# Kernel tuning notes

Hardware: AMD Instinct MI355X
Metric: run time of the kernel (lower is better)

The kernel has to match this reference:

```python
import jax, jax.numpy as jnp
import numpy as np

ALPHA = 2.0    # ATan surrogate sharpness
V_TH = 1.0     # LIF firing threshold
TAU = 2.0      # LIF membrane time constant
BN_EPS = 1e-5
NUM_HEADS = 8

@jax.custom_vjp
def spike(u):
    return (u >= 0.0).astype(u.dtype)

def _spike_fwd(u):
    return spike(u), u

def _spike_bwd(u, g):
    s = (jnp.pi / 2.0) * ALPHA * u
    return (g * (ALPHA / 2.0) / (1.0 + s * s),)

spike.defvjp(_spike_fwd, _spike_bwd)

def lif(x):
    # x: (T, ...) -> binary spikes, multi-step LIF with hard reset
    def step(mem, xt):
        mem = mem + (xt - mem) / TAU
        s = spike(mem - V_TH)
        return mem * (1.0 - s), s
    _, out = jax.lax.scan(step, jnp.zeros_like(x[0]), x)
    return out

def bn_eval(y, bn):
    g, be, m, v = bn[0], bn[1], bn[2], bn[3]  # each (C,)
    return (y - m) * jax.lax.rsqrt(v + BN_EPS) * g + be

def linear_bn_lif(x, W, b, bn):
    # x: (T,B,N,C); W: (C_out, C_in) torch convention
    y = jnp.einsum('tbnc,dc->tbnd', x, W) + b
    return lif(bn_eval(y, bn))

def setup_inputs() -> dict:
    key = jax.random.key(0)
    ks = jax.random.split(key, 6)
    T, B, N, C = 4, 8, 1024, 512
    scale = 1.0 / np.sqrt(C)
    x = jax.random.normal(ks[0], (T, B, N, C), dtype=jnp.float32)
    Wq = jax.random.normal(ks[1], (C, C), dtype=jnp.float32) * scale
    Wk = jax.random.normal(ks[2], (C, C), dtype=jnp.float32) * scale
    Wv = jax.random.normal(ks[3], (C, C), dtype=jnp.float32) * scale
    Wp = jax.random.normal(ks[4], (C, C), dtype=jnp.float32) * scale
    zeros = jnp.zeros((C,), dtype=jnp.float32)
    ones = jnp.ones((C,), dtype=jnp.float32)
    # bn_params[l] = (gamma, beta, running_mean, running_var) for q_bn,k_bn,v_bn,proj_bn
    bn_one = jnp.stack([ones, zeros, zeros, ones])  # (4, C)
    bn_params = jnp.tile(bn_one[None], (4, 1, 1))   # (4, 4, C)
    return {"x": x, "Wq": Wq, "bq": zeros, "Wk": Wk, "bk": zeros,
            "Wv": Wv, "bv": zeros, "Wp": Wp, "bp": zeros, "bn_params": bn_params}

def reference(x, Wq, bq, Wk, bk, Wv, bv, Wp, bp, bn_params):
    T, B, N, C = x.shape
    H = NUM_HEADS
    D = C // H
    q = linear_bn_lif(x, Wq, bq, bn_params[0])
    k = linear_bn_lif(x, Wk, bk, bn_params[1])
    v = linear_bn_lif(x, Wv, bv, bn_params[2])
    # (T,B,N,C) -> (T,B,H,N,D)
    q = q.reshape(T, B, N, H, D).transpose(0, 1, 3, 2, 4)
    k = k.reshape(T, B, N, H, D).transpose(0, 1, 3, 2, 4)
    v = v.reshape(T, B, N, H, D).transpose(0, 1, 3, 2, 4)
    # attention_linear variant: kv = (k^T @ v) / n; y = q @ kv
    # SparseMatmul's tile-sparsity fallback computes the same dense matmul math.
    kv = jnp.einsum('tbhnd,tbhne->tbhde', k, v) / float(N)
    y = jnp.einsum('tbhnd,tbhde->tbhne', q, kv)
    y = y.transpose(0, 1, 3, 2, 4).reshape(T, B, N, C)
    y = lif(y)  # attn_lif
    # final projection: proj -> proj_bn -> proj_lif
    y = jnp.einsum('tbnc,dc->tbnd', y, Wp) + bp
    y = bn_eval(y, bn_params[3])
    y = lif(y)  # proj_lif
    return y
```

## Files before the change

### kernel.cpp

```cpp
#include <hip/hip_runtime.h>
#include <hip/hip_bf16.h>

constexpr int T_ = 4, B_ = 8, N_ = 1024, C_ = 512, H_ = 8, D_ = 64;
constexpr int M_ = 8192;
constexpr int MT_ = 32768;
constexpr int K_ = 512;

#define TAU_INV 0.5f
#define V_TH    1.0f
#define BN_EPS  1e-5f

__device__ __forceinline__ void ld4(const float* p, float* d) {
  const float4 v = *(const float4*)p;
  d[0] = v.x; d[1] = v.y; d[2] = v.z; d[3] = v.w;
}
__device__ __forceinline__ void ld4(const __hip_bfloat16* p, float* d) {
  const ushort4 u = *(const ushort4*)p;
  d[0] = __bfloat162float(*(const __hip_bfloat16*)&u.x);
  d[1] = __bfloat162float(*(const __hip_bfloat16*)&u.y);
  d[2] = __bfloat162float(*(const __hip_bfloat16*)&u.z);
  d[3] = __bfloat162float(*(const __hip_bfloat16*)&u.w);
}
__device__ __forceinline__ void st4(__hip_bfloat16* p, const float* s) {
  ushort4 u;
  *(__hip_bfloat16*)&u.x = __float2bfloat16(s[0]);
  *(__hip_bfloat16*)&u.y = __float2bfloat16(s[1]);
  *(__hip_bfloat16*)&u.z = __float2bfloat16(s[2]);
  *(__hip_bfloat16*)&u.w = __float2bfloat16(s[3]);
  *(ushort4*)p = u;
}
__device__ __forceinline__ void st4(float* p, const float* s) {
  *(float4*)p = make_float4(s[0], s[1], s[2], s[3]);
}

__device__ __forceinline__ void dma16(const void* g, void* l) {
  __builtin_amdgcn_global_load_lds(
      (const __attribute__((address_space(1))) unsigned int*)g,
      (__attribute__((address_space(3))) unsigned int*)l, 16, 0, 0);
}

struct WPtrs { const float* W[4]; };

__global__ __launch_bounds__(256) void transpose_w(WPtrs wp, float* __restrict__ Wt)
{
  __shared__ float tile[32][33];
  const int w = blockIdx.z;
  const float* __restrict__ W = wp.W[w];
  float* __restrict__ dst = Wt + (size_t)w * K_ * C_;
  const int k0 = blockIdx.x * 32, d0 = blockIdx.y * 32;
  const int tx = threadIdx.x, ty = threadIdx.y;
#pragma unroll
  for (int i = 0; i < 32; i += 8)
    tile[ty + i][tx] = W[(size_t)(d0 + ty + i) * K_ + k0 + tx];
  __syncthreads();
#pragma unroll
  for (int i = 0; i < 32; i += 8)
    dst[(size_t)(k0 + ty + i) * C_ + d0 + tx] = tile[tx][ty + i];
}

__global__ __launch_bounds__(256) void transpose_x(
    const float* __restrict__ x, float* __restrict__ XT)
{
  __shared__ float tile[32][132];
  const int bk = blockIdx.x * 32, bm = blockIdx.y * 32;
  const int tx = threadIdx.x & 31, ty = threadIdx.x >> 5;
#pragma unroll
  for (int t = 0; t < T_; ++t)
#pragma unroll
    for (int i = 0; i < 4; ++i) {
      const int m = ty + 8 * i;
      tile[tx][m * 4 + t] = x[((size_t)t * M_ + bm + m) * K_ + bk + tx];
    }
  __syncthreads();
  const int k = threadIdx.x >> 3, q = threadIdx.x & 7;
#pragma unroll
  for (int u = 0; u < 4; ++u)
    st4(&XT[(size_t)(bk + k) * MT_ + bm * 4 + q * 16 + u * 4],
        &tile[k][q * 16 + u * 4]);
}

template <typename TIn, typename TOut>
struct GArgs {
  const TIn* AT;
  const float* Wt[3];
  const float* bias[3];
  const float* bn[3];
  TOut* S[3];
};

template <typename TIn, typename TOut>
__global__ __launch_bounds__(256, 2) void gemm_lif(GArgs<TIn, TOut> args)
{
  constexpr int BK = 32;
  constexpr bool BF = (sizeof(TIn) == 2);
  __shared__ __align__(16) TIn  As[BK * 128];
  __shared__ __align__(16) float Bs[BK * 256];

  const int z = blockIdx.z;
  const TIn*   __restrict__ AT   = args.AT;
  const float* __restrict__ Wt   = args.Wt[z];
  const float* __restrict__ bias = args.bias[z];
  const float* __restrict__ bnp  = args.bn[z];
  TOut*        __restrict__ S    = args.S[z];

  const int tid  = threadIdx.x;
  const int lane = tid & 63;
  const int wave = __builtin_amdgcn_readfirstlane(tid >> 6);
  const int tx = tid & 15, ty = tid >> 4;
  const int bm_m = blockIdx.y * 32;
  const int bm4  = bm_m * 4;
  const int bn0  = blockIdx.x * 256;

  float acc[2][4][4][4];
#pragma unroll
  for (int g = 0; g < 2; ++g)
#pragma unroll
    for (int h = 0; h < 4; ++h)
#pragma unroll
      for (int i = 0; i < 4; ++i)
#pragma unroll
        for (int j = 0; j < 4; ++j) acc[g][h][i][j] = 0.0f;

  for (int k0 = 0; k0 < K_; k0 += BK) {
    if constexpr (!BF) {
#pragma unroll
      for (int c = 0; c < 4; ++c) {
        const int ins = wave * 4 + c;
        const int kk = ins * 2 + (lane >> 5);
        dma16(AT + (size_t)(k0 + kk) * MT_ + bm4 + (lane & 31) * 4,
              (void*)((float*)As + ins * 256));
      }
    } else {
#pragma unroll
      for (int c = 0; c < 2; ++c) {
        const int ins = wave * 2 + c;
        const int kk = ins * 4 + (lane >> 4);
        dma16(AT + (size_t)(k0 + kk) * MT_ + bm4 + (lane & 15) * 8,
              (void*)((TIn*)As + ins * 512));
      }
    }
#pragma unroll
    for (int c = 0; c < 8; ++c) {
      const int ins = wave * 8 + c;
      dma16(Wt + (size_t)(k0 + ins) * C_ + bn0 + lane * 4,
            (void*)(Bs + ins * 256));
    }
    __syncthreads();

#pragma unroll
    for (int kk = 0; kk < BK; ++kk) {
      float a[2][4], b[4][4];
#pragma unroll
      for (int g = 0; g < 2; ++g)
        ld4((const TIn*)As + kk * 128 + ty * 4 + 64 * g, a[g]);
#pragma unroll
      for (int h = 0; h < 4; ++h)
        ld4(Bs + kk * 256 + tx * 4 + 64 * h, b[h]);
#pragma unroll
      for (int g = 0; g < 2; ++g)
#pragma unroll
        for (int h = 0; h < 4; ++h)
#pragma unroll
          for (int i = 0; i < 4; ++i)
#pragma unroll
            for (int j = 0; j < 4; ++j)
              acc[g][h][i][j] += a[g][i] * b[h][j];
    }
    __syncthreads();
  }

#pragma unroll
  for (int h = 0; h < 4; ++h) {
    const int d = bn0 + tx * 4 + 64 * h;
    float bi[4], gg[4], be[4], mu[4], vv[4];
    ld4(&bias[d], bi);
    ld4(&bnp[d], gg);
    ld4(&bnp[C_ + d], be);
    ld4(&bnp[2 * C_ + d], mu);
    ld4(&bnp[3 * C_ + d], vv);
    float inv[4];
#pragma unroll
    for (int j = 0; j < 4; ++j) inv[j] = 1.0f / sqrtf(vv[j] + BN_EPS);
#pragma unroll
    for (int g = 0; g < 2; ++g) {
      const int m = bm_m + ty + 16 * g;
      float sv[4][4];
#pragma unroll
      for (int j = 0; j < 4; ++j) {
        float mm = 0.0f;
#pragma unroll
        for (int t = 0; t < 4; ++t) {
          float y = acc[g][h][t][j] + bi[j];
          y = (y - mu[j]) * inv[j] * gg[j] + be[j];
          float m2 = mm + (y - mm) * TAU_INV;
          float s = (m2 - V_TH >= 0.0f) ? 1.0f : 0.0f;
          sv[t][j] = s;
          mm = (s != 0.0f) ? 0.0f : m2;
        }
      }
#pragma unroll
      for (int t = 0; t < 4; ++t)
        st4(&S[((size_t)t * M_ + m) * C_ + d], sv[t]);
    }
  }
}

__global__ __launch_bounds__(256) void lif_T(
    const float* __restrict__ Y, __hip_bfloat16* __restrict__ AT)
{
  __shared__ __hip_bfloat16 lds[64][72];
  const int bm = blockIdx.x * 16, bc = blockIdx.y * 64;
  const int tid = threadIdx.x;
  const int mm = tid >> 4, c4 = (tid & 15) * 4;
  float mem[4] = {0.0f, 0.0f, 0.0f, 0.0f};
#pragma unroll
  for (int t = 0; t < T_; ++t) {
    float y[4];
    ld4(&Y[((size_t)t * M_ + bm + mm) * C_ + bc + c4], y);
#pragma unroll
    for (int j = 0; j < 4; ++j) {
      float m2 = mem[j] + (y[j] - mem[j]) * TAU_INV;
      float s = (m2 - V_TH >= 0.0f) ? 1.0f : 0.0f;
      lds[c4 + j][mm * 4 + t] = __float2bfloat16(s);
      mem[j] = (s != 0.0f) ? 0.0f : m2;
    }
  }
  __syncthreads();
  const int c = tid >> 2, q = tid & 3;
  *(uint4*)(AT + (size_t)(bc + c) * MT_ + bm * 4 + q * 16) =
      *(const uint4*)&lds[c][q * 16];
}

__global__ __launch_bounds__(256) void attn_kernel(
    const __hip_bfloat16* __restrict__ Q,
    const __hip_bfloat16* __restrict__ Kk,
    const __hip_bfloat16* __restrict__ V,
    float* __restrict__ Y)
{
  __shared__ float s1[64][65];
  __shared__ float s2[64][65];
  __shared__ float kv[64][65];
  const int tid = threadIdx.x;
  const int h = blockIdx.x, b = blockIdx.y, t = blockIdx.z;
  const size_t base = ((size_t)t * B_ + b) * (size_t)N_ * C_ + (size_t)h * D_;
  const int d0 = (tid >> 4) * 4;
  const int e0 = (tid & 15) * 4;

  float acc[4][4];
#pragma unroll
  for (int i = 0; i < 4; ++i)
#pragma unroll
    for (int j = 0; j < 4; ++j) acc[i][j] = 0.0f;

  for (int nc = 0; nc < N_; nc += 64) {
#pragma unroll
    for (int i = 0; i < 16; ++i) {
      int idx = tid + i * 256;
      int r = idx >> 6, c = idx & 63;
      s1[r][c] = __bfloat162float(Kk[base + (size_t)(nc + r) * C_ + c]);
      s2[r][c] = __bfloat162float(V[base + (size_t)(nc + r) * C_ + c]);
    }
    __syncthreads();
#pragma unroll
    for (int nn = 0; nn < 64; ++nn) {
      float a[4], bb[4];
#pragma unroll
      for (int i = 0; i < 4; ++i) a[i] = s1[nn][d0 + i];
#pragma unroll
      for (int j = 0; j < 4; ++j) bb[j] = s2[nn][e0 + j];
#pragma unroll
      for (int i = 0; i < 4; ++i)
#pragma unroll
        for (int j = 0; j < 4; ++j) acc[i][j] += a[i] * bb[j];
    }
    __syncthreads();
  }
#pragma unroll
  for (int i = 0; i < 4; ++i)
#pragma unroll
    for (int j = 0; j < 4; ++j)
      kv[d0 + i][e0 + j] = acc[i][j] * (1.0f / (float)N_);
  __syncthreads();

  for (int rc = 0; rc < N_; rc += 64) {
#pragma unroll
    for (int i = 0; i < 16; ++i) {
      int idx = tid + i * 256;
      int r = idx >> 6, c = idx & 63;
      s1[r][c] = __bfloat162float(Q[base + (size_t)(rc + r) * C_ + c]);
    }
    __syncthreads();
    float o[4][4];
#pragma unroll
    for (int i = 0; i < 4; ++i)
#pragma unroll
      for (int j = 0; j < 4; ++j) o[i][j] = 0.0f;
#pragma unroll
    for (int d = 0; d < 64; ++d) {
      float a[4], bb[4];
#pragma unroll
      for (int i = 0; i < 4; ++i) a[i] = s1[d0 + i][d];
#pragma unroll
      for (int j = 0; j < 4; ++j) bb[j] = kv[d][e0 + j];
#pragma unroll
      for (int i = 0; i < 4; ++i)
#pragma unroll
        for (int j = 0; j < 4; ++j) o[i][j] += a[i] * bb[j];
    }
#pragma unroll
    for (int i = 0; i < 4; ++i)
#pragma unroll
      for (int j = 0; j < 4; ++j)
        Y[base + (size_t)(rc + d0 + i) * C_ + e0 + j] = o[i][j];
    __syncthreads();
  }
}

extern "C" void kernel_launch(void* const* d_in, const int* in_sizes, int n_in,
                              void* d_out, int out_size, void* d_ws, size_t ws_size,
                              hipStream_t stream)
{
  const float* x   = (const float*)d_in[0];
  const float* Wq  = (const float*)d_in[1];
  const float* bq  = (const float*)d_in[2];
  const float* Wk  = (const float*)d_in[3];
  const float* bk  = (const float*)d_in[4];
  const float* Wv  = (const float*)d_in[5];
  const float* bv  = (const float*)d_in[6];
  const float* Wp  = (const float*)d_in[7];
  const float* bp  = (const float*)d_in[8];
  const float* bnp = (const float*)d_in[9];
  float* out = (float*)d_out;

  char* ws = (char*)d_ws;
  float* XT = (float*)ws;  ws += (size_t)K_ * MT_ * sizeof(float);
  float* Wt = (float*)ws;  ws += (size_t)4 * K_ * C_ * sizeof(float);
  __hip_bfloat16* q_s = (__hip_bfloat16*)ws; ws += (size_t)MT_ * C_ * 2;
  __hip_bfloat16* k_s = (__hip_bfloat16*)ws; ws += (size_t)MT_ * C_ * 2;
  __hip_bfloat16* v_s = (__hip_bfloat16*)ws; ws += (size_t)MT_ * C_ * 2;
  float* Y = XT;
  __hip_bfloat16* aT = q_s;

  WPtrs wp; wp.W[0] = Wq; wp.W[1] = Wk; wp.W[2] = Wv; wp.W[3] = Wp;
  transpose_w<<<dim3(K_ / 32, C_ / 32, 4), dim3(32, 8), 0, stream>>>(wp, Wt);
  transpose_x<<<dim3(K_ / 32, M_ / 32), 256, 0, stream>>>(x, XT);

  GArgs<float, __hip_bfloat16> qa;
  qa.AT = XT;
  qa.Wt[0] = Wt; qa.Wt[1] = Wt + (size_t)K_ * C_; qa.Wt[2] = Wt + (size_t)2 * K_ * C_;
  qa.bias[0] = bq; qa.bias[1] = bk; qa.bias[2] = bv;
  qa.bn[0] = bnp + 0 * 4 * C_;
  qa.bn[1] = bnp + 1 * 4 * C_;
  qa.bn[2] = bnp + 2 * 4 * C_;
  qa.S[0] = q_s; qa.S[1] = k_s; qa.S[2] = v_s;
  gemm_lif<float, __hip_bfloat16>
      <<<dim3(C_ / 256, M_ / 32, 3), 256, 0, stream>>>(qa);

  attn_kernel<<<dim3(H_, B_, T_), 256, 0, stream>>>(q_s, k_s, v_s, Y);
  lif_T<<<dim3(M_ / 16, C_ / 64), 256, 0, stream>>>(Y, aT);

  GArgs<__hip_bfloat16, float> pa;
  pa.AT = aT;
  pa.Wt[0] = Wt + (size_t)3 * K_ * C_;
  pa.bias[0] = bp;
  pa.bn[0] = bnp + 3 * 4 * C_;
  pa.S[0] = out;
  gemm_lif<__hip_bfloat16, float>
      <<<dim3(C_ / 256, M_ / 32, 1), 256, 0, stream>>>(pa);
}
```

Before: 984.4 us.

## Double-buffer GEMM shared tiles and vectorize attention bf16 loads

```diff
diff --git a/kernel.cpp b/kernel.cpp
--- a/kernel.cpp
+++ b/kernel.cpp
@@ -91,10 +91,11 @@
 template <typename TIn, typename TOut>
 __global__ __launch_bounds__(256, 2) void gemm_lif(GArgs<TIn, TOut> args)
 {
-  constexpr int BK = 32;
+  constexpr int BK = 16;
+  constexpr int NIT = K_ / BK;
   constexpr bool BF = (sizeof(TIn) == 2);
-  __shared__ __align__(16) TIn  As[BK * 128];
-  __shared__ __align__(16) float Bs[BK * 256];
+  __shared__ __align__(16) TIn  As[2][BK * 128];
+  __shared__ __align__(16) float Bs[2][BK * 256];
 
   const int z = blockIdx.z;
   const TIn*   __restrict__ AT   = args.AT;
@@ -121,41 +122,51 @@
 #pragma unroll
         for (int j = 0; j < 4; ++j) acc[g][h][i][j] = 0.0f;
 
-  for (int k0 = 0; k0 < K_; k0 += BK) {
+  auto stageA = [&](int it) {
+    const int k0 = it * BK;
+    TIn* dst = As[it & 1];
     if constexpr (!BF) {
 #pragma unroll
-      for (int c = 0; c < 4; ++c) {
-        const int ins = wave * 4 + c;
+      for (int c = 0; c < 2; ++c) {
+        const int ins = wave * 2 + c;
         const int kk = ins * 2 + (lane >> 5);
         dma16(AT + (size_t)(k0 + kk) * MT_ + bm4 + (lane & 31) * 4,
-              (void*)((float*)As + ins * 256));
+              (void*)((float*)dst + ins * 256));
       }
     } else {
-#pragma unroll
-      for (int c = 0; c < 2; ++c) {
-        const int ins = wave * 2 + c;
-        const int kk = ins * 4 + (lane >> 4);
-        dma16(AT + (size_t)(k0 + kk) * MT_ + bm4 + (lane & 15) * 8,
-              (void*)((TIn*)As + ins * 512));
-      }
-    }
-#pragma unroll
-    for (int c = 0; c < 8; ++c) {
-      const int ins = wave * 8 + c;
+      const int kk = wave * 4 + (lane >> 4);
+      dma16(AT + (size_t)(k0 + kk) * MT_ + bm4 + (lane & 15) * 8,
+            (void*)((TIn*)dst + wave * 512));
+    }
+  };
+  auto stageB = [&](int it) {
+    const int k0 = it * BK;
+    float* dst = Bs[it & 1];
+#pragma unroll
+    for (int c = 0; c < 4; ++c) {
+      const int ins = wave * 4 + c;
       dma16(Wt + (size_t)(k0 + ins) * C_ + bn0 + lane * 4,
-            (void*)(Bs + ins * 256));
-    }
-    __syncthreads();
+            (void*)(dst + ins * 256));
+    }
+  };
+
+  stageA(0); stageB(0);
+  __syncthreads();
+
+  for (int it = 0; it < NIT; ++it) {
+    if (it + 1 < NIT) { stageA(it + 1); stageB(it + 1); }
+    const TIn*   Ac = As[it & 1];
+    const float* Bc = Bs[it & 1];
 
 #pragma unroll
     for (int kk = 0; kk < BK; ++kk) {
       float a[2][4], b[4][4];
 #pragma unroll
       for (int g = 0; g < 2; ++g)
-        ld4((const TIn*)As + kk * 128 + ty * 4 + 64 * g, a[g]);
+        ld4(Ac + kk * 128 + ty * 4 + 64 * g, a[g]);
 #pragma unroll
       for (int h = 0; h < 4; ++h)
-        ld4(Bs + kk * 256 + tx * 4 + 64 * h, b[h]);
+        ld4(Bc + kk * 256 + tx * 4 + 64 * h, b[h]);
 #pragma unroll
       for (int g = 0; g < 2; ++g)
 #pragma unroll
@@ -254,11 +265,14 @@
 
   for (int nc = 0; nc < N_; nc += 64) {
 #pragma unroll
-    for (int i = 0; i < 16; ++i) {
-      int idx = tid + i * 256;
-      int r = idx >> 6, c = idx & 63;
-      s1[r][c] = __bfloat162float(Kk[base + (size_t)(nc + r) * C_ + c]);
-      s2[r][c] = __bfloat162float(V[base + (size_t)(nc + r) * C_ + c]);
+    for (int i = 0; i < 4; ++i) {
+      const int idx = tid + i * 256;
+      const int r = idx >> 4, c4 = (idx & 15) * 4;
+      float fk[4], fv[4];
+      ld4(&Kk[base + (size_t)(nc + r) * C_ + c4], fk);
+      ld4(&V [base + (size_t)(nc + r) * C_ + c4], fv);
+#pragma unroll
+      for (int j = 0; j < 4; ++j) { s1[r][c4 + j] = fk[j]; s2[r][c4 + j] = fv[j]; }
     }
     __syncthreads();
 #pragma unroll
@@ -284,10 +298,13 @@
 
   for (int rc = 0; rc < N_; rc += 64) {
 #pragma unroll
-    for (int i = 0; i < 16; ++i) {
-      int idx = tid + i * 256;
-      int r = idx >> 6, c = idx & 63;
-      s1[r][c] = __bfloat162float(Q[base + (size_t)(rc + r) * C_ + c]);
+    for (int i = 0; i < 4; ++i) {
+      const int idx = tid + i * 256;
+      const int r = idx >> 4, c4 = (idx & 15) * 4;
+      float fq[4];
+      ld4(&Q[base + (size_t)(rc + r) * C_ + c4], fq);
+#pragma unroll
+      for (int j = 0; j < 4; ++j) s1[r][c4 + j] = fq[j];
     }
     __syncthreads();
     float o[4][4];
```

Result: slower. 1.424 ms (+44.6%).
